# Kernel tuning notes

Measured on AMD Instinct MI355X. Metric: run time of the kernel, lower is better.

## Reference

```python
import jax, jax.numpy as jnp
import numpy as np
import math

D_MODEL = 768
N_HEAD = 12
SEQ_LEN = 2048
BATCH = 4


def setup_inputs() -> dict:
    key = jax.random.key(0)
    ks = jax.random.split(key, 5)
    x = jax.random.normal(ks[0], (BATCH, SEQ_LEN, D_MODEL), dtype=jnp.float32)
    s = 1.0 / math.sqrt(D_MODEL)
    W_attn = jax.random.uniform(ks[1], (D_MODEL, 3 * D_MODEL), minval=-s, maxval=s, dtype=jnp.float32)
    b_attn = jax.random.uniform(ks[2], (3 * D_MODEL,), minval=-s, maxval=s, dtype=jnp.float32)
    W_proj = jax.random.uniform(ks[3], (D_MODEL, D_MODEL), minval=-s, maxval=s, dtype=jnp.float32)
    b_proj = jax.random.uniform(ks[4], (D_MODEL,), minval=-s, maxval=s, dtype=jnp.float32)
    return {"x": x, "W_attn": W_attn, "b_attn": b_attn, "W_proj": W_proj, "b_proj": b_proj}


def reference(x, W_attn, b_attn, W_proj, b_proj):
    B, T, C = x.shape
    H = N_HEAD
    hd = C // H
    qkv = x @ W_attn + b_attn  # [B,T,3C]
    q, k, v = jnp.split(qkv, 3, axis=-1)
    # [B,H,T,hd]
    q = q.reshape(B, T, H, hd).transpose(0, 2, 1, 3)
    k = k.reshape(B, T, H, hd).transpose(0, 2, 1, 3)
    v = v.reshape(B, T, H, hd).transpose(0, 2, 1, 3)
    att = jnp.einsum('bhqd,bhkd->bhqk', q, k) * (1.0 / math.sqrt(hd))  # [B,H,T,T]
    causal = jnp.tril(jnp.ones((T, T), dtype=bool))
    att = jnp.where(causal[None, None, :, :], att, -jnp.inf)
    att = jax.nn.softmax(att, axis=-1)
    # attn_pdrop = resid_pdrop = 0.0 -> dropout is identity
    y = jnp.einsum('bhqk,bhkd->bhqd', att, v)  # [B,H,T,hd]
    y = y.transpose(0, 2, 1, 3).reshape(B, T, C)
    return y @ W_proj + b_proj
```

## Files before the change

### kernel.cpp

```cpp
#include <hip/hip_runtime.h>
#include <hip/hip_bf16.h>
#include <math.h>

#define D_MODEL 768
#define N_HEAD  12
#define SEQ     2048
#define BATCH   4
#define HD      64
#define BH      (BATCH*N_HEAD)

typedef __bf16 bf16;
typedef __bf16 bf16x4 __attribute__((ext_vector_type(4)));
typedef __bf16 bf16x8 __attribute__((ext_vector_type(8)));
typedef float  f32x4  __attribute__((ext_vector_type(4)));
typedef unsigned int u32;

__device__ __forceinline__ f32x4 mfma16(bf16x8 a, bf16x8 b, f32x4 c) {
    return __builtin_amdgcn_mfma_f32_16x16x32_bf16(a, b, c, 0, 0, 0);
}

__device__ __forceinline__ void gload16(const void* g, void* l) {
    __builtin_amdgcn_global_load_lds((const __attribute__((address_space(1))) u32*)g,
                                     (__attribute__((address_space(3))) u32*)l, 16, 0, 0);
}

__global__ void cvt_bf16(const float* __restrict__ in, bf16* __restrict__ out, int n) {
    int i = (blockIdx.x * blockDim.x + threadIdx.x) * 4;
    if (i < n) {
        float4 v = *(const float4*)(in + i);
        bf16x4 o;
        o[0] = (bf16)v.x; o[1] = (bf16)v.y; o[2] = (bf16)v.z; o[3] = (bf16)v.w;
        *(bf16x4*)(out + i) = o;
    }
}

__global__ __launch_bounds__(256)
void transpose_cvt(const float* __restrict__ in, bf16* __restrict__ out, int R, int C) {
    __shared__ float tile[64][65];
    int tid = threadIdx.x;
    int tr = blockIdx.y * 64, tc = blockIdx.x * 64;
    int r0 = tid >> 4, c0 = (tid & 15) * 4;
    #pragma unroll
    for (int i = 0; i < 4; ++i) {
        float4 v = *(const float4*)&in[(long)(tr + r0 + i * 16) * C + tc + c0];
        tile[r0 + i * 16][c0 + 0] = v.x;
        tile[r0 + i * 16][c0 + 1] = v.y;
        tile[r0 + i * 16][c0 + 2] = v.z;
        tile[r0 + i * 16][c0 + 3] = v.w;
    }
    __syncthreads();
    int orr = (tid & 15) * 4;
    #pragma unroll
    for (int i = 0; i < 4; ++i) {
        int oc = (tid >> 4) + i * 16;
        bf16x4 o;
        #pragma unroll
        for (int j = 0; j < 4; ++j) o[j] = (bf16)tile[orr + j][oc];
        *(bf16x4*)&out[(long)(tc + oc) * R + tr + orr] = o;
    }
}

template<int MODE>
__global__ __launch_bounds__(256)
void gemm_bt(const bf16* __restrict__ A, const bf16* __restrict__ Bt,
             const float* __restrict__ bias,
             bf16* __restrict__ qo, bf16* __restrict__ ko, bf16* __restrict__ vto,
             float* __restrict__ outf,
             int M, int N, int K) {
    __shared__ bf16 As[128 * 32];
    __shared__ bf16 Bs[128 * 32];
    int tid = threadIdx.x;
    int wave = tid >> 6, lane = tid & 63;
    int wr = wave >> 1, wc = wave & 1;
    int lq = lane >> 4, lc = lane & 15;
    int mbase = blockIdx.x * 128, nbase = blockIdx.y * 128;
    int srow = wave * 32 + (lane >> 2), scol = (lane & 3) * 8;
    const bf16* aS = A  + (long)(mbase + srow) * K + scol;
    const bf16* bS = Bt + (long)(nbase + srow) * K + scol;
    char* AsB = (char*)As + wave * 2048;
    char* BsB = (char*)Bs + wave * 2048;
    f32x4 acc[4][4] = {};
    for (int kt = 0; kt < K; kt += 32) {
        gload16(aS + kt,                AsB);
        gload16(aS + 16 * (long)K + kt, AsB + 1024);
        gload16(bS + kt,                BsB);
        gload16(bS + 16 * (long)K + kt, BsB + 1024);
        __syncthreads();
        bf16x8 af[4], bfr[4];
        #pragma unroll
        for (int mf = 0; mf < 4; ++mf)
            af[mf]  = *(const bf16x8*)((char*)As + (wr * 64 + mf * 16 + lc) * 64 + lq * 16);
        #pragma unroll
        for (int nf = 0; nf < 4; ++nf)
            bfr[nf] = *(const bf16x8*)((char*)Bs + (wc * 64 + nf * 16 + lc) * 64 + lq * 16);
        __builtin_amdgcn_s_setprio(1);
        #pragma unroll
        for (int mf = 0; mf < 4; ++mf)
            #pragma unroll
            for (int nf = 0; nf < 4; ++nf)
                acc[mf][nf] = mfma16(af[mf], bfr[nf], acc[mf][nf]);
        __builtin_amdgcn_s_setprio(0);
        __syncthreads();
    }
    #pragma unroll
    for (int mf = 0; mf < 4; ++mf) {
        #pragma unroll
        for (int nf = 0; nf < 4; ++nf) {
            int n = nbase + wc * 64 + nf * 16 + lc;
            float bv = bias[n];
            int m0 = mbase + wr * 64 + mf * 16 + lq * 4;
            if (MODE == 0) {
                int sect = n / 768, cc = n % 768;
                int h = cc >> 6, d = cc & 63;
                int b = m0 >> 11, t0 = m0 & 2047;
                long bh = (long)b * N_HEAD + h;
                if (sect == 0) {
                    #pragma unroll
                    for (int r = 0; r < 4; ++r)
                        qo[(bh * SEQ + t0 + r) * HD + d] = (bf16)((acc[mf][nf][r] + bv) * 0.125f);
                } else if (sect == 1) {
                    #pragma unroll
                    for (int r = 0; r < 4; ++r)
                        ko[(bh * SEQ + t0 + r) * HD + d] = (bf16)(acc[mf][nf][r] + bv);
                } else {
                    bf16x4 o;
                    #pragma unroll
                    for (int r = 0; r < 4; ++r) o[r] = (bf16)(acc[mf][nf][r] + bv);
                    *(bf16x4*)&vto[(bh * HD + d) * SEQ + t0] = o;
                }
            } else {
                #pragma unroll
                for (int r = 0; r < 4; ++r)
                    outf[(long)(m0 + r) * N + n] = acc[mf][nf][r] + bv;
            }
        }
    }
}

__global__ __launch_bounds__(256, 4)
void attn_kernel(const bf16* __restrict__ qg, const bf16* __restrict__ kg,
                 const bf16* __restrict__ vtg, bf16* __restrict__ yg) {
    __shared__ bf16 Ks[64 * 64];
    __shared__ bf16 Vs[64 * 64];
    __shared__ bf16 Ps[4][16][72];
    int tid = threadIdx.x;
    int wave = tid >> 6, lane = tid & 63;
    int lq = lane >> 4, lc = lane & 15;
    int qb = gridDim.x - 1 - blockIdx.x;
    int bh = blockIdx.y;
    int b = bh / N_HEAD, h = bh % N_HEAD;
    long koff = (long)bh * SEQ * HD;
    long voff = (long)bh * HD * SEQ;
    int q0 = qb * 128 + wave * 16 + lc;
    int q1 = q0 + 64;

    int srow0 = wave * 16 + (lane >> 3);
    int scolsw = ((lane & 7) ^ (lane >> 3)) << 3;

    bf16x8 qfA[2], qfB[2];
    qfA[0] = *(const bf16x8*)&qg[koff + (long)q0 * HD + lq * 8];
    qfA[1] = *(const bf16x8*)&qg[koff + (long)q0 * HD + 32 + lq * 8];
    qfB[0] = *(const bf16x8*)&qg[koff + (long)q1 * HD + lq * 8];
    qfB[1] = *(const bf16x8*)&qg[koff + (long)q1 * HD + 32 + lq * 8];

    f32x4 yA[4] = {}, yB[4] = {};
    float mA = -INFINITY, lsA = 0.f, mB = -INFINITY, lsB = 0.f;
    const float L2E = 1.4426950408889634f;
    int swz = (lane & 7) << 3;
    const char* KsC = (const char*)Ks;
    const char* VsC = (const char*)Vs;
    int k0 = 0;

    auto half = [&](const bf16x8* qf, int qrow, bool diag,
                    float& m2, float& lsum, f32x4* yacc) {
        f32x4 st[4];
        __builtin_amdgcn_s_setprio(1);
        #pragma unroll
        for (int sub = 0; sub < 4; ++sub) {
            bf16x8 kf0 = *(const bf16x8*)(KsC + ((sub * 16 + lc) * 64 + ((lq * 8) ^ swz)) * 2);
            bf16x8 kf1 = *(const bf16x8*)(KsC + ((sub * 16 + lc) * 64 + ((32 + lq * 8) ^ swz)) * 2);
            f32x4 s = {};
            s = mfma16(kf0, qf[0], s);
            s = mfma16(kf1, qf[1], s);
            st[sub] = s;
        }
        __builtin_amdgcn_s_setprio(0);
        float pmax = -INFINITY;
        if (diag) {
            #pragma unroll
            for (int sub = 0; sub < 4; ++sub)
                #pragma unroll
                for (int r = 0; r < 4; ++r) {
                    int k = k0 + sub * 16 + lq * 4 + r;
                    if (k > qrow) st[sub][r] = -INFINITY;
                    pmax = fmaxf(pmax, st[sub][r]);
                }
        } else {
            #pragma unroll
            for (int sub = 0; sub < 4; ++sub)
                #pragma unroll
                for (int r = 0; r < 4; ++r) pmax = fmaxf(pmax, st[sub][r]);
        }
        pmax = fmaxf(pmax, __shfl_xor(pmax, 16));
        pmax = fmaxf(pmax, __shfl_xor(pmax, 32));
        if (!__all(pmax <= m2 + 5.5452f)) {
            float mnew = fmaxf(m2, pmax);
            float sc = __builtin_amdgcn_exp2f((m2 - mnew) * L2E);
            #pragma unroll
            for (int dt = 0; dt < 4; ++dt) yacc[dt] *= sc;
            lsum *= sc;
            m2 = mnew;
        }
        float m2L = m2 * L2E;
        float psum = 0.f;
        #pragma unroll
        for (int sub = 0; sub < 4; ++sub) {
            bf16x4 pk;
            #pragma unroll
            for (int r = 0; r < 4; ++r) {
                float p = __builtin_amdgcn_exp2f(__builtin_fmaf(st[sub][r], L2E, -m2L));
                psum += p;
                pk[r] = (bf16)p;
            }
            *(bf16x4*)&Ps[wave][lc][sub * 16 + lq * 4] = pk;
        }
        psum += __shfl_xor(psum, 16);
        psum += __shfl_xor(psum, 32);
        lsum += psum;
        bf16x8 pf0 = *(const bf16x8*)&Ps[wave][lc][lq * 8];
        bf16x8 pf1 = *(const bf16x8*)&Ps[wave][lc][32 + lq * 8];
        __builtin_amdgcn_s_setprio(1);
        #pragma unroll
        for (int dt = 0; dt < 4; ++dt) {
            bf16x8 v0 = *(const bf16x8*)(VsC + ((dt * 16 + lc) * 64 + ((lq * 8) ^ swz)) * 2);
            bf16x8 v1 = *(const bf16x8*)(VsC + ((dt * 16 + lc) * 64 + ((32 + lq * 8) ^ swz)) * 2);
            yacc[dt] = mfma16(v0, pf0, yacc[dt]);
            yacc[dt] = mfma16(v1, pf1, yacc[dt]);
        }
        __builtin_amdgcn_s_setprio(0);
    };

    int nkt = 2 * qb + 2;
    for (int kt = 0; kt < nkt; ++kt) {
        k0 = kt * 64;
        {
            char* KsB = (char*)Ks + wave * 2048;
            char* VsB = (char*)Vs + wave * 2048;
            gload16(kg + koff + (long)(k0 + srow0) * HD + scolsw,       KsB);
            gload16(kg + koff + (long)(k0 + srow0 + 8) * HD + scolsw,   KsB + 1024);
            gload16(vtg + voff + (long)srow0 * SEQ + k0 + scolsw,       VsB);
            gload16(vtg + voff + (long)(srow0 + 8) * SEQ + k0 + scolsw, VsB + 1024);
        }
        __syncthreads();
        if (kt <= 2 * qb) half(qfA, q0, kt == 2 * qb, mA, lsA, yA);
        half(qfB, q1, kt == nkt - 1, mB, lsB, yB);
        __syncthreads();
    }

    float invA = 1.f / lsA, invB = 1.f / lsB;
    long rowA = ((long)b * SEQ + q0) * D_MODEL + (long)h * HD;
    long rowB = ((long)b * SEQ + q1) * D_MODEL + (long)h * HD;
    #pragma unroll
    for (int dt = 0; dt < 4; ++dt) {
        bf16x4 oA, oB;
        #pragma unroll
        for (int r = 0; r < 4; ++r) {
            oA[r] = (bf16)(yA[dt][r] * invA);
            oB[r] = (bf16)(yB[dt][r] * invB);
        }
        *(bf16x4*)&yg[rowA + dt * 16 + lq * 4] = oA;
        *(bf16x4*)&yg[rowB + dt * 16 + lq * 4] = oB;
    }
}

extern "C" void kernel_launch(void* const* d_in, const int* in_sizes, int n_in,
                              void* d_out, int out_size, void* d_ws, size_t ws_size,
                              hipStream_t stream) {
    const float* x      = (const float*)d_in[0];
    const float* W_attn = (const float*)d_in[1];
    const float* b_attn = (const float*)d_in[2];
    const float* W_proj = (const float*)d_in[3];
    const float* b_proj = (const float*)d_in[4];
    float* out = (float*)d_out;

    char* ws = (char*)d_ws;
    size_t off = 0;
    auto alloc = [&](size_t bytes) { void* p = ws + off; off += (bytes + 255) & ~255ULL; return p; };
    bf16* xb  = (bf16*)alloc(8192ULL * 768 * 2);
    bf16* Wab = (bf16*)alloc(2304ULL * 768 * 2);
    bf16* Wpb = (bf16*)alloc(768ULL * 768 * 2);
    bf16* qb_ = (bf16*)alloc((size_t)BH * SEQ * HD * 2);
    bf16* kb_ = (bf16*)alloc((size_t)BH * SEQ * HD * 2);
    bf16* vtb = (bf16*)alloc((size_t)BH * SEQ * HD * 2);
    bf16* yb  = (bf16*)alloc(8192ULL * 768 * 2);

    hipLaunchKernelGGL(cvt_bf16, dim3((8192 * 768 / 4 + 255) / 256), dim3(256), 0, stream,
                       x, xb, 8192 * 768);
    hipLaunchKernelGGL(transpose_cvt, dim3(2304 / 64, 768 / 64), dim3(256), 0, stream,
                       W_attn, Wab, 768, 2304);
    hipLaunchKernelGGL(transpose_cvt, dim3(768 / 64, 768 / 64), dim3(256), 0, stream,
                       W_proj, Wpb, 768, 768);
    hipLaunchKernelGGL((gemm_bt<0>), dim3(64, 18), dim3(256), 0, stream,
                       xb, Wab, b_attn, qb_, kb_, vtb, (float*)nullptr, 8192, 2304, 768);
    hipLaunchKernelGGL(attn_kernel, dim3(16, 48), dim3(256), 0, stream,
                       qb_, kb_, vtb, yb);
    hipLaunchKernelGGL((gemm_bt<1>), dim3(64, 6), dim3(256), 0, stream,
                       yb, Wpb, b_proj, (bf16*)nullptr, (bf16*)nullptr, (bf16*)nullptr, out, 8192, 768, 768);
}
```

Measured before the change: 237.9 us.

## Rewrite attention with 32x32 MFMA, register-resident P, and paired causal tiles

The attention kernel moves from 16x16x32 to 32x32x16 bf16 MFMA. Each wave now owns 32 query rows, and the softmax probabilities are passed between lanes with cross-lane shuffles instead of a round trip through LDS. Blocks pair a low and a high causal query tile (j and 31-j) so every block has the same amount of work, and the grid is reordered with batch-head as the fast index. The log2(e) factor is folded into the Q scaling in the QKV GEMM epilogue, which removes a multiply per score. The costs are more registers per thread (launch bounds drop to 3 blocks per CU) and extra shuffle traffic, and the lazy rescale threshold is widened.

```diff
diff --git a/kernel.cpp b/kernel.cpp
--- a/kernel.cpp
+++ b/kernel.cpp
@@ -13,10 +13,14 @@
 typedef __bf16 bf16x4 __attribute__((ext_vector_type(4)));
 typedef __bf16 bf16x8 __attribute__((ext_vector_type(8)));
 typedef float  f32x4  __attribute__((ext_vector_type(4)));
+typedef float  f32x16 __attribute__((ext_vector_type(16)));
 typedef unsigned int u32;
 
 __device__ __forceinline__ f32x4 mfma16(bf16x8 a, bf16x8 b, f32x4 c) {
     return __builtin_amdgcn_mfma_f32_16x16x32_bf16(a, b, c, 0, 0, 0);
+}
+__device__ __forceinline__ f32x16 mfma32(bf16x8 a, bf16x8 b, f32x16 c) {
+    return __builtin_amdgcn_mfma_f32_32x32x16_bf16(a, b, c, 0, 0, 0);
 }
 
 __device__ __forceinline__ void gload16(const void* g, void* l) {
@@ -117,7 +121,7 @@
                 if (sect == 0) {
                     #pragma unroll
                     for (int r = 0; r < 4; ++r)
-                        qo[(bh * SEQ + t0 + r) * HD + d] = (bf16)((acc[mf][nf][r] + bv) * 0.125f);
+                        qo[(bh * SEQ + t0 + r) * HD + d] = (bf16)((acc[mf][nf][r] + bv) * 0.18033688f);
                 } else if (sect == 1) {
                     #pragma unroll
                     for (int r = 0; r < 4; ++r)
@@ -137,112 +141,40 @@
     }
 }
 
-__global__ __launch_bounds__(256, 4)
+__global__ __launch_bounds__(256, 3)
 void attn_kernel(const bf16* __restrict__ qg, const bf16* __restrict__ kg,
                  const bf16* __restrict__ vtg, bf16* __restrict__ yg) {
     __shared__ bf16 Ks[64 * 64];
     __shared__ bf16 Vs[64 * 64];
-    __shared__ bf16 Ps[4][16][72];
     int tid = threadIdx.x;
     int wave = tid >> 6, lane = tid & 63;
-    int lq = lane >> 4, lc = lane & 15;
-    int qb = gridDim.x - 1 - blockIdx.x;
-    int bh = blockIdx.y;
-    int b = bh / N_HEAD, h = bh % N_HEAD;
+    int q5 = lane & 31, h = lane >> 5;
+    int bh = blockIdx.x, j = blockIdx.y;
+    int b = bh / N_HEAD, hh = bh % N_HEAD;
+    int wp = wave >> 1;
+    int myt     = wp ? 31 - j : j;
+    int mytiles = wp ? 32 - j : j + 1;
+    int nkt = 32 - j;
     long koff = (long)bh * SEQ * HD;
     long voff = (long)bh * HD * SEQ;
-    int q0 = qb * 128 + wave * 16 + lc;
-    int q1 = q0 + 64;
+    int qrow = myt * 64 + (wave & 1) * 32 + q5;
+
+    bf16x8 qf[4];
+    #pragma unroll
+    for (int s = 0; s < 4; ++s)
+        qf[s] = *(const bf16x8*)&qg[koff + (long)qrow * HD + s * 16 + h * 8];
+
+    f32x16 y0 = {}, y1 = {};
+    float m2 = -INFINITY, lsum = 0.f;
 
     int srow0 = wave * 16 + (lane >> 3);
     int scolsw = ((lane & 7) ^ (lane >> 3)) << 3;
-
-    bf16x8 qfA[2], qfB[2];
-    qfA[0] = *(const bf16x8*)&qg[koff + (long)q0 * HD + lq * 8];
-    qfA[1] = *(const bf16x8*)&qg[koff + (long)q0 * HD + 32 + lq * 8];
-    qfB[0] = *(const bf16x8*)&qg[koff + (long)q1 * HD + lq * 8];
-    qfB[1] = *(const bf16x8*)&qg[koff + (long)q1 * HD + 32 + lq * 8];
-
-    f32x4 yA[4] = {}, yB[4] = {};
-    float mA = -INFINITY, lsA = 0.f, mB = -INFINITY, lsB = 0.f;
-    const float L2E = 1.4426950408889634f;
-    int swz = (lane & 7) << 3;
+    int rsw = lane & 7;
     const char* KsC = (const char*)Ks;
     const char* VsC = (const char*)Vs;
-    int k0 = 0;
-
-    auto half = [&](const bf16x8* qf, int qrow, bool diag,
-                    float& m2, float& lsum, f32x4* yacc) {
-        f32x4 st[4];
-        __builtin_amdgcn_s_setprio(1);
-        #pragma unroll
-        for (int sub = 0; sub < 4; ++sub) {
-            bf16x8 kf0 = *(const bf16x8*)(KsC + ((sub * 16 + lc) * 64 + ((lq * 8) ^ swz)) * 2);
-            bf16x8 kf1 = *(const bf16x8*)(KsC + ((sub * 16 + lc) * 64 + ((32 + lq * 8) ^ swz)) * 2);
-            f32x4 s = {};
-            s = mfma16(kf0, qf[0], s);
-            s = mfma16(kf1, qf[1], s);
-            st[sub] = s;
-        }
-        __builtin_amdgcn_s_setprio(0);
-        float pmax = -INFINITY;
-        if (diag) {
-            #pragma unroll
-            for (int sub = 0; sub < 4; ++sub)
-                #pragma unroll
-                for (int r = 0; r < 4; ++r) {
-                    int k = k0 + sub * 16 + lq * 4 + r;
-                    if (k > qrow) st[sub][r] = -INFINITY;
-                    pmax = fmaxf(pmax, st[sub][r]);
-                }
-        } else {
-            #pragma unroll
-            for (int sub = 0; sub < 4; ++sub)
-                #pragma unroll
-                for (int r = 0; r < 4; ++r) pmax = fmaxf(pmax, st[sub][r]);
-        }
-        pmax = fmaxf(pmax, __shfl_xor(pmax, 16));
-        pmax = fmaxf(pmax, __shfl_xor(pmax, 32));
-        if (!__all(pmax <= m2 + 5.5452f)) {
-            float mnew = fmaxf(m2, pmax);
-            float sc = __builtin_amdgcn_exp2f((m2 - mnew) * L2E);
-            #pragma unroll
-            for (int dt = 0; dt < 4; ++dt) yacc[dt] *= sc;
-            lsum *= sc;
-            m2 = mnew;
-        }
-        float m2L = m2 * L2E;
-        float psum = 0.f;
-        #pragma unroll
-        for (int sub = 0; sub < 4; ++sub) {
-            bf16x4 pk;
-            #pragma unroll
-            for (int r = 0; r < 4; ++r) {
-                float p = __builtin_amdgcn_exp2f(__builtin_fmaf(st[sub][r], L2E, -m2L));
-                psum += p;
-                pk[r] = (bf16)p;
-            }
-            *(bf16x4*)&Ps[wave][lc][sub * 16 + lq * 4] = pk;
-        }
-        psum += __shfl_xor(psum, 16);
-        psum += __shfl_xor(psum, 32);
-        lsum += psum;
-        bf16x8 pf0 = *(const bf16x8*)&Ps[wave][lc][lq * 8];
-        bf16x8 pf1 = *(const bf16x8*)&Ps[wave][lc][32 + lq * 8];
-        __builtin_amdgcn_s_setprio(1);
-        #pragma unroll
-        for (int dt = 0; dt < 4; ++dt) {
-            bf16x8 v0 = *(const bf16x8*)(VsC + ((dt * 16 + lc) * 64 + ((lq * 8) ^ swz)) * 2);
-            bf16x8 v1 = *(const bf16x8*)(VsC + ((dt * 16 + lc) * 64 + ((32 + lq * 8) ^ swz)) * 2);
-            yacc[dt] = mfma16(v0, pf0, yacc[dt]);
-            yacc[dt] = mfma16(v1, pf1, yacc[dt]);
-        }
-        __builtin_amdgcn_s_setprio(0);
-    };
-
-    int nkt = 2 * qb + 2;
+
     for (int kt = 0; kt < nkt; ++kt) {
-        k0 = kt * 64;
+        int k0 = kt * 64;
         {
             char* KsB = (char*)Ks + wave * 2048;
             char* VsB = (char*)Vs + wave * 2048;
@@ -252,24 +184,100 @@
             gload16(vtg + voff + (long)(srow0 + 8) * SEQ + k0 + scolsw, VsB + 1024);
         }
         __syncthreads();
-        if (kt <= 2 * qb) half(qfA, q0, kt == 2 * qb, mA, lsA, yA);
-        half(qfB, q1, kt == nkt - 1, mB, lsB, yB);
+        if (kt < mytiles) {
+            f32x16 s0 = {}, s1 = {};
+            __builtin_amdgcn_s_setprio(1);
+            #pragma unroll
+            for (int s = 0; s < 4; ++s) {
+                bf16x8 kf0 = *(const bf16x8*)(KsC + q5 * 128        + (((s * 2 + h) ^ rsw) << 4));
+                bf16x8 kf1 = *(const bf16x8*)(KsC + (32 + q5) * 128 + (((s * 2 + h) ^ rsw) << 4));
+                s0 = mfma32(kf0, qf[s], s0);
+                s1 = mfma32(kf1, qf[s], s1);
+            }
+            __builtin_amdgcn_s_setprio(0);
+            if (kt == mytiles - 1) {
+                #pragma unroll
+                for (int r = 0; r < 16; ++r) {
+                    int ka = k0 + (r & 3) + 8 * (r >> 2) + 4 * h;
+                    if (ka > qrow)      s0[r] = -INFINITY;
+                    if (ka + 32 > qrow) s1[r] = -INFINITY;
+                }
+            }
+            float pmax = s0[0];
+            #pragma unroll
+            for (int r = 1; r < 16; ++r) pmax = fmaxf(pmax, s0[r]);
+            #pragma unroll
+            for (int r = 0; r < 16; ++r) pmax = fmaxf(pmax, s1[r]);
+            pmax = fmaxf(pmax, __shfl_xor(pmax, 32));
+            if (!__all(pmax <= m2 + 11.5f)) {
+                float mnew = fmaxf(m2, pmax);
+                float sc = __builtin_amdgcn_exp2f(m2 - mnew);
+                #pragma unroll
+                for (int r = 0; r < 16; ++r) { y0[r] *= sc; y1[r] *= sc; }
+                lsum *= sc;
+                m2 = mnew;
+            }
+            float psum = 0.f;
+            u32 d0a[4], d1a[4], d0b[4], d1b[4];
+            #pragma unroll
+            for (int m = 0; m < 4; ++m) {
+                union { bf16x4 v; u32 w[2]; } pa, pb;
+                #pragma unroll
+                for (int rr = 0; rr < 4; ++rr) {
+                    float p0 = __builtin_amdgcn_exp2f(s0[4 * m + rr] - m2);
+                    float p1 = __builtin_amdgcn_exp2f(s1[4 * m + rr] - m2);
+                    psum += p0 + p1;
+                    pa.v[rr] = (bf16)p0; pb.v[rr] = (bf16)p1;
+                }
+                d0a[m] = pa.w[0]; d1a[m] = pa.w[1];
+                d0b[m] = pb.w[0]; d1b[m] = pb.w[1];
+            }
+            psum += __shfl_xor(psum, 32);
+            lsum += psum;
+            u32 e0a[4], e1a[4], e0b[4], e1b[4];
+            #pragma unroll
+            for (int m = 0; m < 4; ++m) {
+                e0a[m] = __shfl_xor(d0a[m], 32); e1a[m] = __shfl_xor(d1a[m], 32);
+                e0b[m] = __shfl_xor(d0b[m], 32); e1b[m] = __shfl_xor(d1b[m], 32);
+            }
+            __builtin_amdgcn_s_setprio(1);
+            #pragma unroll
+            for (int s = 0; s < 4; ++s) {
+                int m0 = 2 * (s & 1), m1 = m0 + 1;
+                union { bf16x8 v; u32 w[4]; } fr;
+                if (s < 2) {
+                    fr.w[0] = h ? e0a[m1] : d0a[m0];
+                    fr.w[1] = h ? e1a[m1] : d1a[m0];
+                    fr.w[2] = h ? d0a[m1] : e0a[m0];
+                    fr.w[3] = h ? d1a[m1] : e1a[m0];
+                } else {
+                    fr.w[0] = h ? e0b[m1] : d0b[m0];
+                    fr.w[1] = h ? e1b[m1] : d1b[m0];
+                    fr.w[2] = h ? d0b[m1] : e0b[m0];
+                    fr.w[3] = h ? d1b[m1] : e1b[m0];
+                }
+                bf16x8 v0 = *(const bf16x8*)(VsC + q5 * 128        + (((s * 2 + h) ^ rsw) << 4));
+                bf16x8 v1 = *(const bf16x8*)(VsC + (32 + q5) * 128 + (((s * 2 + h) ^ rsw) << 4));
+                y0 = mfma32(v0, fr.v, y0);
+                y1 = mfma32(v1, fr.v, y1);
+            }
+            __builtin_amdgcn_s_setprio(0);
+        }
         __syncthreads();
     }
 
-    float invA = 1.f / lsA, invB = 1.f / lsB;
-    long rowA = ((long)b * SEQ + q0) * D_MODEL + (long)h * HD;
-    long rowB = ((long)b * SEQ + q1) * D_MODEL + (long)h * HD;
-    #pragma unroll
-    for (int dt = 0; dt < 4; ++dt) {
-        bf16x4 oA, oB;
-        #pragma unroll
-        for (int r = 0; r < 4; ++r) {
-            oA[r] = (bf16)(yA[dt][r] * invA);
-            oB[r] = (bf16)(yB[dt][r] * invB);
+    float inv = 1.f / lsum;
+    long rowoff = ((long)b * SEQ + qrow) * D_MODEL + (long)hh * HD;
+    #pragma unroll
+    for (int m = 0; m < 4; ++m) {
+        bf16x4 o0, o1;
+        #pragma unroll
+        for (int rr = 0; rr < 4; ++rr) {
+            o0[rr] = (bf16)(y0[4 * m + rr] * inv);
+            o1[rr] = (bf16)(y1[4 * m + rr] * inv);
         }
-        *(bf16x4*)&yg[rowA + dt * 16 + lq * 4] = oA;
-        *(bf16x4*)&yg[rowB + dt * 16 + lq * 4] = oB;
+        *(bf16x4*)&yg[rowoff + 8 * m + 4 * h]      = o0;
+        *(bf16x4*)&yg[rowoff + 32 + 8 * m + 4 * h] = o1;
     }
 }
 
@@ -302,7 +310,7 @@
                        W_proj, Wpb, 768, 768);
     hipLaunchKernelGGL((gemm_bt<0>), dim3(64, 18), dim3(256), 0, stream,
                        xb, Wab, b_attn, qb_, kb_, vtb, (float*)nullptr, 8192, 2304, 768);
-    hipLaunchKernelGGL(attn_kernel, dim3(16, 48), dim3(256), 0, stream,
+    hipLaunchKernelGGL(attn_kernel, dim3(48, 16), dim3(256), 0, stream,
                        qb_, kb_, vtb, yb);
     hipLaunchKernelGGL((gemm_bt<1>), dim3(64, 6), dim3(256), 0, stream,
                        yb, Wpb, b_proj, (bf16*)nullptr, (bf16*)nullptr, (bf16*)nullptr, out, 8192, 768, 768);
```

Measured after the change: 211.1 us. -11.3%, faster.
